# Kernel tuning notes

Measured on AMD Instinct MI355X. Metric: run time of the kernel, lower is better.

The kernel has to match this reference:

```python
import jax, jax.numpy as jnp
import numpy as np

IMAGE_SIZE = 512
STRIDES = (8, 16, 32)
W_SEG, W_DET, W_CLS = 1.0, 1.0, 0.5


def _bce_logits(x, y):
    # numerically stable binary cross entropy with logits (broadcasts y)
    return jnp.maximum(x, 0.0) - x * y + jnp.log1p(jnp.exp(-jnp.abs(x)))


def _focal_loss_mean(logits, targets, num_classes, alpha=0.25, gamma=2.0):
    # sigmoid focal loss; targets are class indices, -1 (or any negative) => all-background row
    t = jax.nn.one_hot(targets, num_classes, dtype=logits.dtype)
    p = jax.nn.sigmoid(logits)
    ce = _bce_logits(logits, t)
    p_t = p * t + (1.0 - p) * (1.0 - t)
    a_t = alpha * t + (1.0 - alpha) * (1.0 - t)
    return jnp.mean(a_t * (1.0 - p_t) ** gamma * ce)


def _det_scale_loss(cls_logits, reg_preds, cent_preds, boxes, labels, stride):
    B, Cp1, H, W = cls_logits.shape
    C = Cp1 - 1
    L = H * W
    cls = jnp.transpose(cls_logits, (0, 2, 3, 1))[..., 1:].reshape(B, L, C)
    reg = jnp.transpose(reg_preds, (0, 2, 3, 1)).reshape(B, L, 4)
    cent = cent_preds.reshape(B, L)
    xs = (jnp.arange(W, dtype=jnp.float32) + 0.5) * stride
    ys = (jnp.arange(H, dtype=jnp.float32) + 0.5) * stride
    gy, gx = jnp.meshgrid(ys, xs, indexing='ij')
    loc_x = gx.reshape(-1)
    loc_y = gy.reshape(-1)

    def per_image(cls_i, reg_i, cent_i, gb, gl):
        b = gb * IMAGE_SIZE  # [cx,cy,w,h] in pixels
        x0 = b[:, 0] - b[:, 2] * 0.5
        y0 = b[:, 1] - b[:, 3] * 0.5
        x1 = b[:, 0] + b[:, 2] * 0.5
        y1 = b[:, 1] + b[:, 3] * 0.5
        l = loc_x[:, None] - x0[None, :]
        t = loc_y[:, None] - y0[None, :]
        r = x1[None, :] - loc_x[:, None]
        btm = y1[None, :] - loc_y[:, None]
        ltrb = jnp.stack([l, t, r, btm], axis=-1)  # (L, N, 4)
        inside = jnp.min(ltrb, axis=-1) > 0
        area = (x1 - x0) * (y1 - y0)
        masked_area = jnp.where(inside, area[None, :], jnp.inf)
        idx = jnp.argmin(masked_area, axis=-1)  # min-area matched box per location
        pos = jnp.any(inside, axis=-1)
        cls_t = jnp.where(pos, gl[idx], -1)
        reg_t = jnp.take_along_axis(ltrb, idx[:, None, None], axis=1)[:, 0, :] / stride
        lr = reg_t[:, jnp.array([0, 2])]
        tb = reg_t[:, jnp.array([1, 3])]
        eps = 1e-6
        cen_t = jnp.sqrt(jnp.clip((jnp.min(lr, -1) / (jnp.max(lr, -1) + eps)) * (jnp.min(tb, -1) / (jnp.max(tb, -1) + eps)), 0.0, 1.0))
        cls_l = _focal_loss_mean(cls_i, cls_t, C)
        npos = jnp.sum(pos)
        d = reg_i - reg_t
        sl1 = jnp.mean(jnp.where(jnp.abs(d) < 1.0, 0.5 * d * d, jnp.abs(d) - 0.5), axis=-1)
        posf = pos.astype(jnp.float32)
        denom = jnp.maximum(npos, 1).astype(jnp.float32)
        reg_l = jnp.where(npos > 0, jnp.sum(sl1 * posf) / denom, 0.0)
        bce = _bce_logits(cent_i, cen_t)
        cen_l = jnp.where(npos > 0, jnp.sum(bce * posf) / denom, 0.0)
        return cls_l, reg_l, cen_l

    cl, rl, cel = jax.vmap(per_image)(cls, reg, cent, boxes, labels)
    return jnp.mean(cl), jnp.mean(rl), jnp.mean(cel)


def _total_loss(seg_logits, seg_mask, cls_list, reg_list, cen_list, boxes, labels, cls_pred, cls_target):
    # segmentation: BCE-with-logits, integer mask broadcast as float target over channels
    seg_t = seg_mask.astype(jnp.float32)[:, None, :, :]  # (B,1,H,W) broadcasts vs (B,C,H,W)
    seg_loss = jnp.mean(_bce_logits(seg_logits, seg_t))
    tot_cls = 0.0
    tot_reg = 0.0
    tot_cen = 0.0
    for s in range(3):
        cl, rl, cel = _det_scale_loss(cls_list[s], reg_list[s], cen_list[s], boxes, labels, STRIDES[s])
        tot_cls = tot_cls + cl
        tot_reg = tot_reg + rl
        tot_cen = tot_cen + cel
    n = 3.0
    det_loss = tot_cls / n + tot_reg / n + tot_cen / n
    cls_loss = _focal_loss_mean(cls_pred, cls_target, cls_pred.shape[-1])
    return W_SEG * seg_loss + W_DET * det_loss + W_CLS * cls_loss


def setup_inputs() -> dict:
    key = jax.random.key(0)
    ks = jax.random.split(key, 16)
    B = 32
    inp = {
        'seg_logits': jax.random.normal(ks[0], (B, 4, 512, 512), jnp.float32),
        'seg_mask': jax.random.randint(ks[1], (B, 512, 512), 0, 4, jnp.int32),
        'cls_logits_s0': jax.random.normal(ks[2], (B, 5, 64, 64), jnp.float32),
        'cls_logits_s1': jax.random.normal(ks[3], (B, 5, 32, 32), jnp.float32),
        'cls_logits_s2': jax.random.normal(ks[4], (B, 5, 16, 16), jnp.float32),
        'reg_preds_s0': jax.random.normal(ks[5], (B, 4, 64, 64), jnp.float32),
        'reg_preds_s1': jax.random.normal(ks[6], (B, 4, 32, 32), jnp.float32),
        'reg_preds_s2': jax.random.normal(ks[7], (B, 4, 16, 16), jnp.float32),
        'centerness_s0': jax.random.normal(ks[8], (B, 1, 64, 64), jnp.float32),
        'centerness_s1': jax.random.normal(ks[9], (B, 1, 32, 32), jnp.float32),
        'centerness_s2': jax.random.normal(ks[10], (B, 1, 16, 16), jnp.float32),
        'boxes': jax.random.uniform(ks[11], (B, 20, 4), jnp.float32),
        'labels': jax.random.randint(ks[12], (B, 20), 0, 4, jnp.int32),
        'cls_pred': jax.random.normal(ks[13], (B, 10), jnp.float32),
        'cls_target': jax.random.randint(ks[14], (B,), 0, 10, jnp.int32),
    }
    return inp


def reference(seg_logits, seg_mask, cls_logits_s0, cls_logits_s1, cls_logits_s2, reg_preds_s0, reg_preds_s1, reg_preds_s2, centerness_s0, centerness_s1, centerness_s2, boxes, labels, cls_pred, cls_target):
    return _total_loss(seg_logits, seg_mask,
                       (cls_logits_s0, cls_logits_s1, cls_logits_s2),
                       (reg_preds_s0, reg_preds_s1, reg_preds_s2),
                       (centerness_s0, centerness_s1, centerness_s2),
                       boxes, labels, cls_pred, cls_target)
```

## Files before the change

kernel.cpp:

```cpp
#include <hip/hip_runtime.h>
#include <math.h>

#define NB 32
#define DET_BLOCKS 96
#define SEG_BLOCKS 2048
#define TOTAL_BLOCKS (DET_BLOCKS + SEG_BLOCKS)
#define SEG_THREADS (SEG_BLOCKS * 256)
#define SEG_QUADS   (NB * 4 * 65536)
#define SEG_ITERS   (SEG_QUADS / SEG_THREADS)

typedef float floatx4 __attribute__((ext_vector_type(4)));
typedef int   intx4   __attribute__((ext_vector_type(4)));


__device__ __forceinline__ float bce_logits(float x, float y) {
    float a = fabsf(x);
    return fmaxf(x, 0.f) - x * y + __logf(1.f + __expf(-a));
}

__device__ __forceinline__ float bce4(floatx4 x, intx4 m) {
    return bce_logits(x.x, (float)m.x) + bce_logits(x.y, (float)m.y)
         + bce_logits(x.z, (float)m.z) + bce_logits(x.w, (float)m.w);
}

__device__ __forceinline__ float focal_elt(float x, float t) {
    float p = 1.f / (1.f + __expf(-x));
    float ce = bce_logits(x, t);
    float p_t = (t > 0.5f) ? p : (1.f - p);
    float a_t = (t > 0.5f) ? 0.25f : 0.75f;
    float om = 1.f - p_t;
    return a_t * om * om * ce;
}

template <int N>
__device__ void blk_reduce_arr(float* v) {
    __shared__ float sm[N][4];
    int lane = threadIdx.x & 63;
    int wid  = threadIdx.x >> 6;
#pragma unroll
    for (int j = 0; j < N; j++) {
        float x = v[j];
#pragma unroll
        for (int off = 32; off > 0; off >>= 1) x += __shfl_down(x, off, 64);
        if (lane == 0) sm[j][wid] = x;
    }
    __syncthreads();
    if (threadIdx.x == 0) {
#pragma unroll
        for (int j = 0; j < N; j++) {
            float s = 0.f;
#pragma unroll
            for (int w = 0; w < 4; w++) s += sm[j][w];
            v[j] = s;
        }
    }
}


__global__ __launch_bounds__(256) void fused_kernel(
        const float* __restrict__ seg_logits, const int* __restrict__ mask,
        const float* __restrict__ cls0, const float* __restrict__ cls1, const float* __restrict__ cls2,
        const float* __restrict__ reg0, const float* __restrict__ reg1, const float* __restrict__ reg2,
        const float* __restrict__ cen0, const float* __restrict__ cen1, const float* __restrict__ cen2,
        const float* __restrict__ boxes, const int* __restrict__ labels,
        float* __restrict__ segpart, float* __restrict__ detc) {

    if (blockIdx.x < DET_BLOCKS) {
        const int s = blockIdx.x >> 5;
        const int b = blockIdx.x & 31;
        int Wd, shift, L; float stride;
        const float *cls, *reg, *cen;
        if (s == 0)      { Wd = 64; shift = 6; L = 4096; stride = 8.f;  cls = cls0; reg = reg0; cen = cen0; }
        else if (s == 1) { Wd = 32; shift = 5; L = 1024; stride = 16.f; cls = cls1; reg = reg1; cen = cen1; }
        else             { Wd = 16; shift = 4; L = 256;  stride = 32.f; cls = cls2; reg = reg2; cen = cen2; }

        __shared__ float sx0[20], sy0[20], sx1[20], sy1[20], sar[20];
        __shared__ int   slb[20];
        if (threadIdx.x < 20) {
            int k = threadIdx.x;
            const float* bb = boxes + (b * 20 + k) * 4;
            float cx = bb[0] * 512.f, cy = bb[1] * 512.f;
            float w  = bb[2] * 512.f, h  = bb[3] * 512.f;
            float x0 = cx - 0.5f * w, y0 = cy - 0.5f * h;
            float x1 = cx + 0.5f * w, y1 = cy + 0.5f * h;
            sx0[k] = x0; sy0[k] = y0; sx1[k] = x1; sy1[k] = y1;
            sar[k] = (x1 - x0) * (y1 - y0);
            slb[k] = labels[b * 20 + k];
        }
        __syncthreads();

        const float* clsb = cls + (size_t)b * 5 * L;
        const float* regb = reg + (size_t)b * 4 * L;
        const float* cenb = cen + (size_t)b * L;
        const float inv = 1.f / stride;

        float cls_s = 0.f, reg_s = 0.f, cen_s = 0.f, np = 0.f;
        for (int l = threadIdx.x; l < L; l += 256) {
            float lx = ((l & (Wd - 1)) + 0.5f) * stride;
            float ly = ((l >> shift)   + 0.5f) * stride;
            int bk = -1; float ba = INFINITY;
            float bl = 0.f, btp = 0.f, brr = 0.f, bbt = 0.f;
#pragma unroll
            for (int k = 0; k < 20; k++) {
                float li = lx - sx0[k], ti = ly - sy0[k];
                float ri = sx1[k] - lx, bi = sy1[k] - ly;
                float mn = fminf(fminf(li, ti), fminf(ri, bi));
                if (mn > 0.f && sar[k] < ba) {
                    ba = sar[k]; bk = k;
                    bl = li; btp = ti; brr = ri; bbt = bi;
                }
            }
            int tl = (bk >= 0) ? slb[bk] : -1;
#pragma unroll
            for (int c = 0; c < 4; c++) {
                float x = clsb[(c + 1) * L + l];
                cls_s += focal_elt(x, (c == tl) ? 1.f : 0.f);
            }
            if (bk >= 0) {
                float r0 = bl * inv, r1 = btp * inv, r2 = brr * inv, r3 = bbt * inv;
                float d0 = regb[0 * L + l] - r0;
                float d1 = regb[1 * L + l] - r1;
                float d2 = regb[2 * L + l] - r2;
                float d3 = regb[3 * L + l] - r3;
                float a0 = fabsf(d0), a1 = fabsf(d1), a2 = fabsf(d2), a3 = fabsf(d3);
                float sl = (a0 < 1.f ? 0.5f * d0 * d0 : a0 - 0.5f)
                         + (a1 < 1.f ? 0.5f * d1 * d1 : a1 - 0.5f)
                         + (a2 < 1.f ? 0.5f * d2 * d2 : a2 - 0.5f)
                         + (a3 < 1.f ? 0.5f * d3 * d3 : a3 - 0.5f);
                reg_s += 0.25f * sl;
                float mnlr = fminf(r0, r2), mxlr = fmaxf(r0, r2);
                float mntb = fminf(r1, r3), mxtb = fmaxf(r1, r3);
                float v = (mnlr / (mxlr + 1e-6f)) * (mntb / (mxtb + 1e-6f));
                v = fminf(fmaxf(v, 0.f), 1.f);
                float ct = sqrtf(v);
                cen_s += bce_logits(cenb[l], ct);
                np += 1.f;
            }
        }

        float v4[4] = {cls_s, reg_s, cen_s, np};
        blk_reduce_arr<4>(v4);
        if (threadIdx.x == 0) {
            float cls_l = v4[0] / (L * 4.f);
            float npos  = v4[3];
            float denom = fmaxf(npos, 1.f);
            float reg_l = (npos > 0.f) ? v4[1] / denom : 0.f;
            float cen_l = (npos > 0.f) ? v4[2] / denom : 0.f;
            detc[blockIdx.x] = (cls_l + reg_l + cen_l) * (1.f / (float)DET_BLOCKS);
        }
        return;
    }

    const int g = (blockIdx.x - DET_BLOCKS) * 256 + threadIdx.x;
    const floatx4* Lq = (const floatx4*)seg_logits;
    const intx4*   Mq = (const intx4*)mask;

    float acc = 0.f;
#pragma unroll 4
    for (int i = 0; i < SEG_ITERS; i++) {
        const int q  = g + i * SEG_THREADS;
        const int mi = ((q >> 18) << 16) | (q & 65535);
        const floatx4 x = Lq[q];
        const intx4   m = Mq[mi];
        acc += bce4(x, m);
    }

    float v[1] = {acc};
    blk_reduce_arr<1>(v);
    if (threadIdx.x == 0) segpart[blockIdx.x - DET_BLOCKS] = v[0];
}


__global__ __launch_bounds__(256) void final_kernel(
        const float* __restrict__ segpart, const float* __restrict__ detc,
        const float* __restrict__ cls_pred, const int* __restrict__ cls_target,
        float* __restrict__ out) {
    const float seg_scale = 1.f / 33554432.f;
    const float cls_scale = 0.5f / 320.f;
    float acc = 0.f;
    for (int i = threadIdx.x; i < SEG_BLOCKS; i += 256) acc += segpart[i] * seg_scale;
    if (threadIdx.x < DET_BLOCKS) acc += detc[threadIdx.x];
    for (int e = threadIdx.x; e < NB * 10; e += 256) {
        int i = e / 10, c = e - i * 10;
        acc += cls_scale * focal_elt(cls_pred[e], (cls_target[i] == c) ? 1.f : 0.f);
    }
    float v[1] = {acc};
    blk_reduce_arr<1>(v);
    if (threadIdx.x == 0) out[0] = v[0];
}


extern "C" void kernel_launch(void* const* d_in, const int* in_sizes, int n_in,
                              void* d_out, int out_size, void* d_ws, size_t ws_size,
                              hipStream_t stream) {
    const float* seg_logits = (const float*)d_in[0];
    const int*   seg_mask   = (const int*)d_in[1];
    const float* cls0 = (const float*)d_in[2];
    const float* cls1 = (const float*)d_in[3];
    const float* cls2 = (const float*)d_in[4];
    const float* reg0 = (const float*)d_in[5];
    const float* reg1 = (const float*)d_in[6];
    const float* reg2 = (const float*)d_in[7];
    const float* cen0 = (const float*)d_in[8];
    const float* cen1 = (const float*)d_in[9];
    const float* cen2 = (const float*)d_in[10];
    const float* boxes  = (const float*)d_in[11];
    const int*   labels = (const int*)d_in[12];
    const float* cls_pred   = (const float*)d_in[13];
    const int*   cls_target = (const int*)d_in[14];

    float* ws      = (float*)d_ws;
    float* segpart = ws;
    float* detc    = ws + SEG_BLOCKS;

    fused_kernel<<<TOTAL_BLOCKS, 256, 0, stream>>>(seg_logits, seg_mask,
                                                   cls0, cls1, cls2,
                                                   reg0, reg1, reg2,
                                                   cen0, cen1, cen2,
                                                   boxes, labels, segpart, detc);
    final_kernel<<<1, 256, 0, stream>>>(segpart, detc, cls_pred, cls_target,
                                        (float*)d_out);
}
```

Measured before the change: 248.4 us.

## Reuse seg mask across channels by remapping seg blocks per image slice

Each seg block now owns one image and a 2048-quad spatial slice. It loads the mask for that slice once into registers, converted to float, and reuses it for all 4 channels of logits. The old code re-read the mask for every channel. This cuts mask traffic and int-to-float conversions, and halves the number of seg blocks, giving fewer, larger blocks and higher register pressure.

```diff
diff --git a/kernel.cpp b/kernel.cpp
--- a/kernel.cpp
+++ b/kernel.cpp
@@ -3,11 +3,8 @@
 
 #define NB 32
 #define DET_BLOCKS 96
-#define SEG_BLOCKS 2048
+#define SEG_BLOCKS 1024
 #define TOTAL_BLOCKS (DET_BLOCKS + SEG_BLOCKS)
-#define SEG_THREADS (SEG_BLOCKS * 256)
-#define SEG_QUADS   (NB * 4 * 65536)
-#define SEG_ITERS   (SEG_QUADS / SEG_THREADS)
 
 typedef float floatx4 __attribute__((ext_vector_type(4)));
 typedef int   intx4   __attribute__((ext_vector_type(4)));
@@ -16,11 +13,6 @@
 __device__ __forceinline__ float bce_logits(float x, float y) {
     float a = fabsf(x);
     return fmaxf(x, 0.f) - x * y + __logf(1.f + __expf(-a));
-}
-
-__device__ __forceinline__ float bce4(floatx4 x, intx4 m) {
-    return bce_logits(x.x, (float)m.x) + bce_logits(x.y, (float)m.y)
-         + bce_logits(x.z, (float)m.z) + bce_logits(x.w, (float)m.w);
 }
 
 __device__ __forceinline__ float focal_elt(float x, float t) {
@@ -151,23 +143,38 @@
         return;
     }
 
-    const int g = (blockIdx.x - DET_BLOCKS) * 256 + threadIdx.x;
-    const floatx4* Lq = (const floatx4*)seg_logits;
-    const intx4*   Mq = (const intx4*)mask;
+    const int s = blockIdx.x - DET_BLOCKS;
+    const int b = s >> 5;
+    const int k = s & 31;
+    const int t = threadIdx.x;
+
+    const intx4*   Mq = (const intx4*)mask + (size_t)b * 65536 + k * 2048;
+    const floatx4* Lq = (const floatx4*)seg_logits + (size_t)b * 262144 + k * 2048;
+
+    intx4 mr[8];
+#pragma unroll
+    for (int j = 0; j < 8; j++) mr[j] = Mq[j * 256 + t];
+    float mf[8][4];
+#pragma unroll
+    for (int j = 0; j < 8; j++) {
+        mf[j][0] = (float)mr[j].x; mf[j][1] = (float)mr[j].y;
+        mf[j][2] = (float)mr[j].z; mf[j][3] = (float)mr[j].w;
+    }
 
     float acc = 0.f;
-#pragma unroll 4
-    for (int i = 0; i < SEG_ITERS; i++) {
-        const int q  = g + i * SEG_THREADS;
-        const int mi = ((q >> 18) << 16) | (q & 65535);
-        const floatx4 x = Lq[q];
-        const intx4   m = Mq[mi];
-        acc += bce4(x, m);
+#pragma unroll
+    for (int c = 0; c < 4; c++) {
+#pragma unroll
+        for (int j = 0; j < 8; j++) {
+            const floatx4 x = Lq[c * 65536 + j * 256 + t];
+            acc += bce_logits(x.x, mf[j][0]) + bce_logits(x.y, mf[j][1])
+                 + bce_logits(x.z, mf[j][2]) + bce_logits(x.w, mf[j][3]);
+        }
     }
 
     float v[1] = {acc};
     blk_reduce_arr<1>(v);
-    if (threadIdx.x == 0) segpart[blockIdx.x - DET_BLOCKS] = v[0];
+    if (threadIdx.x == 0) segpart[s] = v[0];
 }
 
 
```

Result: no change. 248.8 us (+0.2%).
